# Optimization experiments

Hardware: AMD Instinct MI355X
Metric: run time of the kernel (lower is better)

The kernel has to match this reference:

```python
import jax, jax.numpy as jnp
import numpy as np

C_M, C_Z, C_H = 256, 128, 32
S, N = 128, 384
EPS = 1e-5


def setup_inputs() -> dict:
    key = jax.random.key(0)
    ks = jax.random.split(key, 8)
    sc = 1.0 / np.sqrt(C_M)
    return {
        "msa": jax.random.normal(ks[0], (S, N, C_M), dtype=jnp.float32),
        "ln_g": jnp.ones((C_M,), dtype=jnp.float32),
        "ln_b": jnp.zeros((C_M,), dtype=jnp.float32),
        "Wl": jax.random.uniform(ks[1], (C_M, C_H), jnp.float32, -sc, sc),
        "bl": jax.random.uniform(ks[2], (C_H,), jnp.float32, -sc, sc),
        "Wr": jax.random.uniform(ks[3], (C_M, C_H), jnp.float32, -sc, sc),
        "br": jax.random.uniform(ks[4], (C_H,), jnp.float32, -sc, sc),
        "Wo": jax.random.uniform(ks[5], (C_H * C_H, C_Z), jnp.float32, -1.0 / C_H, 1.0 / C_H),
        "bo": jax.random.uniform(ks[6], (C_Z,), jnp.float32, -1.0 / C_H, 1.0 / C_H),
    }


def _layernorm(x, g, b):
    mu = jnp.mean(x, axis=-1, keepdims=True)
    var = jnp.mean(jnp.square(x - mu), axis=-1, keepdims=True)
    return (x - mu) * jax.lax.rsqrt(var + EPS) * g + b


def reference(msa, ln_g, ln_b, Wl, bl, Wr, br, Wo, bo):
    s = msa.shape[0]
    m = _layernorm(msa, ln_g, ln_b)          # [s, n, c_m]
    left = m @ Wl + bl                        # [s, n, c_h]
    right = m @ Wr + br                       # [s, n, c_h]
    outer = jnp.einsum('sic,sjd->ijcd', left, right) / s  # [n, n, c_h, c_h]
    outer = outer.reshape(outer.shape[0], outer.shape[1], -1)
    return outer @ Wo + bo                    # [n, n, c_z]
```

## Files before the change

kernel.cpp:

```cpp
#include <hip/hip_runtime.h>
#include <hip/hip_bf16.h>

#define CM 256
#define CZ 128
#define CH 32
#define SS 128
#define NN 384

typedef short bf16x8 __attribute__((ext_vector_type(8)));
typedef float f32x4 __attribute__((ext_vector_type(4)));
typedef unsigned short us4 __attribute__((ext_vector_type(4)));
typedef unsigned short us8 __attribute__((ext_vector_type(8)));

__device__ __forceinline__ unsigned short f2bf(float f) {
    __hip_bfloat16 h = __float2bfloat16(f);
    return __builtin_bit_cast(unsigned short, h);
}

__device__ __forceinline__ void gl_lds16(const unsigned short* g, unsigned short* l) {
    __builtin_amdgcn_global_load_lds(
        (const __attribute__((address_space(1))) unsigned int*)g,
        (__attribute__((address_space(3))) unsigned int*)l,
        16, 0, 0);
}

__global__ __launch_bounds__(256) void k0_transpose(
    const float* __restrict__ Wo, const float* __restrict__ Wl, const float* __restrict__ Wr,
    unsigned short* __restrict__ WoF, unsigned short* __restrict__ WT) {
    int n = blockIdx.x;
    int base = n * 1024;
#pragma unroll
    for (int u = 0; u < 4; u++) {
        int w   = base + u * 256 + threadIdx.x;
        int e   = w & 7;
        int l   = (w >> 3) & 63;
        int zb  = (w >> 9) & 7;
        int cch = w >> 12;
        WoF[w] = f2bf(Wo[(size_t)(cch * 32 + (l >> 4) * 8 + e) * CZ + zb * 16 + (l & 15)]);
    }
    int k = threadIdx.x;
    if (n < 32) {
        WT[n * CM + k] = f2bf(Wl[(size_t)k * CH + n]);
    } else if (n < 64) {
        WT[32 * CM + (n - 32) * CM + k] = f2bf(Wr[(size_t)k * CH + (n - 32)]);
    }
}

__global__ __launch_bounds__(256, 2) void k1_ln_proj(
    const float* __restrict__ msa, const float* __restrict__ g, const float* __restrict__ bta,
    const unsigned short* __restrict__ WT, const float* __restrict__ bl, const float* __restrict__ br,
    unsigned short* __restrict__ Lt, unsigned short* __restrict__ Rt)
{
    __shared__ unsigned short A_lds[64 * 264];
    __shared__ unsigned short B_lds[64 * 264];

    const int i    = blockIdx.x;
    const int sh   = blockIdx.y;
    const int t    = threadIdx.x;
    const int wv   = t >> 6;
    const int lane = t & 63;
    const int lr   = lane & 15, lg = lane >> 4;

    const float4 gv = ((const float4*)g)[lane];
    const float4 bv = ((const float4*)bta)[lane];
#pragma unroll 4
    for (int r = 0; r < 16; r++) {
        int sl = wv * 16 + r;
        int s  = sh * 64 + sl;
        float4 v = ((const float4*)(msa + ((size_t)s * NN + i) * CM))[lane];
        float sum = v.x + v.y + v.z + v.w;
        float sq  = v.x * v.x + v.y * v.y + v.z * v.z + v.w * v.w;
#pragma unroll
        for (int off = 32; off >= 1; off >>= 1) {
            sum += __shfl_xor(sum, off, 64);
            sq  += __shfl_xor(sq, off, 64);
        }
        float mu = sum * (1.f / CM);
        float rs = rsqrtf(sq * (1.f / CM) - mu * mu + 1e-5f);
        us4 pk;
        pk[0] = f2bf((v.x - mu) * rs * gv.x + bv.x);
        pk[1] = f2bf((v.y - mu) * rs * gv.y + bv.y);
        pk[2] = f2bf((v.z - mu) * rs * gv.z + bv.z);
        pk[3] = f2bf((v.w - mu) * rs * gv.w + bv.w);
        *(us4*)&A_lds[sl * 264 + lane * 4] = pk;
    }
#pragma unroll
    for (int u = 0; u < 8; u++) {
        int id = u * 256 + t;
        *(us8*)&B_lds[(id >> 5) * 264 + (id & 31) * 8] = *(const us8*)&WT[id * 8];
    }
    __syncthreads();

    const int m0 = (wv >> 1) * 32;
    const int n0 = (wv & 1) * 32;
    f32x4 acc[2][2];
#pragma unroll
    for (int a = 0; a < 2; a++)
#pragma unroll
        for (int b = 0; b < 2; b++) acc[a][b] = (f32x4){0.f, 0.f, 0.f, 0.f};

#pragma unroll
    for (int ks = 0; ks < 8; ks++) {
        int ko = ks * 32 + lg * 8;
        bf16x8 a0 = *(const bf16x8*)&A_lds[(m0 + lr) * 264 + ko];
        bf16x8 a1 = *(const bf16x8*)&A_lds[(m0 + 16 + lr) * 264 + ko];
        bf16x8 b0 = *(const bf16x8*)&B_lds[(n0 + lr) * 264 + ko];
        bf16x8 b1 = *(const bf16x8*)&B_lds[(n0 + 16 + lr) * 264 + ko];
        acc[0][0] = __builtin_amdgcn_mfma_f32_16x16x32_bf16(a0, b0, acc[0][0], 0, 0, 0);
        acc[0][1] = __builtin_amdgcn_mfma_f32_16x16x32_bf16(a0, b1, acc[0][1], 0, 0, 0);
        acc[1][0] = __builtin_amdgcn_mfma_f32_16x16x32_bf16(a1, b0, acc[1][0], 0, 0, 0);
        acc[1][1] = __builtin_amdgcn_mfma_f32_16x16x32_bf16(a1, b1, acc[1][1], 0, 0, 0);
    }

    const bool isL = (n0 == 0);
    const float scale = isL ? 0.0078125f : 1.f;
#pragma unroll
    for (int mt = 0; mt < 2; mt++)
#pragma unroll
        for (int nt = 0; nt < 2; nt++) {
            int ch = (n0 + nt * 16 + lr) & 31;
            float bias = isL ? bl[ch] : br[ch];
            us4 pk;
#pragma unroll
            for (int rg = 0; rg < 4; rg++)
                pk[rg] = f2bf((acc[mt][nt][rg] + bias) * scale);
            unsigned short* dst = (isL ? Lt : Rt) + (size_t)(i * CH + ch) * SS
                                  + sh * 64 + m0 + mt * 16 + lg * 4;
            *(us4*)dst = pk;
        }
}

#define TI 8
#define TJ 8
#define P1_B_OFF 65536
#define OH1_OFF  65536
#define K2_LDS   139264

#define FRAG(base, row, o) \
    (*(const bf16x8*)((base) + (((o) & 8) << 11) + (row) * 64 + ((((o) & 7) ^ ((row) & 7)) << 3)))

__global__ __launch_bounds__(512, 2) void k2_fused(
    const unsigned short* __restrict__ Lt, const unsigned short* __restrict__ Rt,
    const unsigned short* __restrict__ WoF, const float* __restrict__ bo,
    float* __restrict__ out)
{
    extern __shared__ char smem[];
    unsigned short* A = (unsigned short*)(smem);
    unsigned short* B = (unsigned short*)(smem + P1_B_OFF);

    const int i0 = blockIdx.x * TI;
    const int j0 = blockIdx.y * TJ;
    const int t  = threadIdx.x;
    const int wv = t >> 6, lane = t & 63;
    const int lr = lane & 15, lg = lane >> 4;

    const unsigned short* gA = Lt + (size_t)i0 * CH * SS;
    const unsigned short* gB = Rt + (size_t)j0 * CH * SS;

    auto stage_half = [&](const unsigned short* gS, unsigned short* lS, int h) {
#pragma unroll
        for (int p = 0; p < 4; p++) {
            int q = wv * 4 + p;
            int d = q * 64 + lane;
            int row = d >> 3, ow = d & 7;
            const unsigned short* src = gS + row * 128 + (h * 8 + (ow ^ (row & 7))) * 8;
            gl_lds16(src, lS + h * 16384 + q * 512);
        }
    };

    stage_half(gA, A, 0);
    stage_half(gB, B, 0);
    asm volatile("s_waitcnt vmcnt(0)" ::: "memory");
    __syncthreads();
    stage_half(gA, A, 1);
    stage_half(gB, B, 1);

    const int m0  = (wv >> 2) * 128;
    const int n0w = (wv & 3) * 64;

    f32x4 accE[4][4], accO[4][4];
#pragma unroll
    for (int a = 0; a < 4; a++)
#pragma unroll
        for (int b = 0; b < 4; b++) {
            accE[a][b] = (f32x4){0.f, 0.f, 0.f, 0.f};
            accO[a][b] = (f32x4){0.f, 0.f, 0.f, 0.f};
        }

#pragma unroll
    for (int ks = 0; ks < 2; ks++) {
        int o = ks * 4 + lg;
        bf16x8 af[8], bfr[4];
#pragma unroll
        for (int mt = 0; mt < 8; mt++) af[mt]  = FRAG(A, m0 + mt * 16 + lr, o);
#pragma unroll
        for (int nt = 0; nt < 4; nt++) bfr[nt] = FRAG(B, n0w + nt * 16 + lr, o);
#pragma unroll
        for (int mt = 0; mt < 8; mt++)
#pragma unroll
            for (int nt = 0; nt < 4; nt++) {
                if (mt & 1)
                    accO[mt >> 1][nt] = __builtin_amdgcn_mfma_f32_16x16x32_bf16(bfr[nt], af[mt], accO[mt >> 1][nt], 0, 0, 0);
                else
                    accE[mt >> 1][nt] = __builtin_amdgcn_mfma_f32_16x16x32_bf16(bfr[nt], af[mt], accE[mt >> 1][nt], 0, 0, 0);
            }
    }
    asm volatile("s_waitcnt vmcnt(0)" ::: "memory");
    __syncthreads();
#pragma unroll
    for (int ks = 2; ks < 4; ks++) {
        int o = ks * 4 + lg;
        bf16x8 af[8], bfr[4];
#pragma unroll
        for (int mt = 0; mt < 8; mt++) af[mt]  = FRAG(A, m0 + mt * 16 + lr, o);
#pragma unroll
        for (int nt = 0; nt < 4; nt++) bfr[nt] = FRAG(B, n0w + nt * 16 + lr, o);
#pragma unroll
        for (int mt = 0; mt < 8; mt++)
#pragma unroll
            for (int nt = 0; nt < 4; nt++) {
                if (mt & 1)
                    accO[mt >> 1][nt] = __builtin_amdgcn_mfma_f32_16x16x32_bf16(bfr[nt], af[mt], accO[mt >> 1][nt], 0, 0, 0);
                else
                    accE[mt >> 1][nt] = __builtin_amdgcn_mfma_f32_16x16x32_bf16(bfr[nt], af[mt], accE[mt >> 1][nt], 0, 0, 0);
            }
    }
    __syncthreads();

    const int zsl = wv & 1, ksl = wv >> 1;

    bf16x8 wbuf[2][4];
#pragma unroll
    for (int bi = 0; bi < 4; bi++)
        wbuf[0][bi] = *(const bf16x8*)&WoF[(((size_t)(0 * 4 + ksl) * 8 + zsl * 4 + bi) * 64 + lane) * 8];
#pragma unroll
    for (int bi = 0; bi < 4; bi++)
        wbuf[1][bi] = *(const bf16x8*)&WoF[(((size_t)(1 * 4 + ksl) * 8 + zsl * 4 + bi) * 64 + lane) * 8];

    {
        unsigned short* Oh0 = (unsigned short*)smem;
        unsigned short* Oh1 = (unsigned short*)(smem + OH1_OFF);
#pragma unroll
        for (int mh = 0; mh < 4; mh++) {
            int iiw  = (wv >> 2) * 4 + mh;
            int rowH = iiw * 16 + lr;
            int okey = (rowH ^ (rowH >> 4)) & 7;
#pragma unroll
            for (int nt = 0; nt < 4; nt++) {
                int colBase = n0w + nt * 16 + lg * 4;
                int chk = (colBase >> 3) ^ okey;
                int off = rowH * 256 + chk * 8 + (lg & 1) * 4;
                us4 pkE, pkO;
#pragma unroll
                for (int rg = 0; rg < 4; rg++) {
                    pkE[rg] = f2bf(accE[mh][nt][rg]);
                    pkO[rg] = f2bf(accO[mh][nt][rg]);
                }
                *(us4*)&Oh0[off] = pkE;
                *(us4*)&Oh1[off] = pkO;
            }
        }
    }
    __syncthreads();

    f32x4 acc2[4][4];
#pragma unroll
    for (int a = 0; a < 4; a++)
#pragma unroll
        for (int b = 0; b < 4; b++) acc2[a][b] = (f32x4){0.f, 0.f, 0.f, 0.f};

#pragma unroll
    for (int c = 0; c < 8; c++) {
        const int cch = c * 4 + ksl;
        const int hh  = cch >> 4;
        const int cH  = cch & 15;
        const unsigned short* OhX = (const unsigned short*)(smem + (hh ? OH1_OFF : 0));

        bf16x8 af2[4];
#pragma unroll
        for (int ai = 0; ai < 4; ai++) {
            int rowH = (ai * 2 + ((lane >> 3) & 1)) * 16 + cH;
            int okey = (rowH ^ (rowH >> 4)) & 7;
            int chk  = (((lane & 7) * 4 + lg) ^ okey);
            af2[ai] = *(const bf16x8*)&OhX[rowH * 256 + chk * 8];
        }
#pragma unroll
        for (int ai = 0; ai < 4; ai++)
#pragma unroll
            for (int bi = 0; bi < 4; bi++)
                acc2[ai][bi] = __builtin_amdgcn_mfma_f32_16x16x32_bf16(af2[ai], wbuf[c & 1][bi], acc2[ai][bi], 0, 0, 0);

        if (c < 6) {
            int cchn = (c + 2) * 4 + ksl;
#pragma unroll
            for (int bi = 0; bi < 4; bi++)
                wbuf[c & 1][bi] = *(const bf16x8*)&WoF[(((size_t)cchn * 8 + zsl * 4 + bi) * 64 + lane) * 8];
        }
    }
    __syncthreads();

    float* RB = (float*)smem;
#pragma unroll
    for (int ai = 0; ai < 4; ai++)
#pragma unroll
        for (int bi = 0; bi < 4; bi++) {
            int z  = zsl * 64 + bi * 16 + lr;
            int pr = ai * 16 + lg * 4;
            *(f32x4*)&RB[ksl * 8704 + z * 68 + pr] = acc2[ai][bi];
        }
    __syncthreads();

    {
        int z = t >> 2, pq = t & 3;
        float bz = bo[z];
#pragma unroll
        for (int u = 0; u < 4; u++) {
            int p0r = pq * 16 + u * 4;
            f32x4 s = (f32x4){0.f, 0.f, 0.f, 0.f};
#pragma unroll
            for (int ks2 = 0; ks2 < 4; ks2++)
                s += *(const f32x4*)&RB[ks2 * 8704 + z * 68 + p0r];
#pragma unroll
            for (int e = 0; e < 4; e++) {
                int p = p0r + e;
                out[((size_t)(i0 + (p >> 3)) * NN + (j0 + (p & 7))) * CZ + z] = s[e] + bz;
            }
        }
    }
}

extern "C" void kernel_launch(void* const* d_in, const int* in_sizes, int n_in,
                              void* d_out, int out_size, void* d_ws, size_t ws_size,
                              hipStream_t stream) {
    const float* msa  = (const float*)d_in[0];
    const float* ln_g = (const float*)d_in[1];
    const float* ln_b = (const float*)d_in[2];
    const float* Wl   = (const float*)d_in[3];
    const float* bl   = (const float*)d_in[4];
    const float* Wr   = (const float*)d_in[5];
    const float* br   = (const float*)d_in[6];
    const float* Wo   = (const float*)d_in[7];
    const float* bo   = (const float*)d_in[8];
    float* out = (float*)d_out;

    unsigned short* Lt  = (unsigned short*)d_ws;
    unsigned short* Rt  = Lt + (size_t)NN * CH * SS;
    unsigned short* WoF = Rt + (size_t)NN * CH * SS;
    unsigned short* WT  = WoF + (size_t)CZ * CH * CH;

    hipFuncSetAttribute((const void*)k2_fused,
                        hipFuncAttributeMaxDynamicSharedMemorySize, K2_LDS);

    k0_transpose<<<dim3(CZ), dim3(256), 0, stream>>>(Wo, Wl, Wr, WoF, WT);
    k1_ln_proj<<<dim3(NN, 2), dim3(256), 0, stream>>>(msa, ln_g, ln_b, WT, bl, br, Lt, Rt);
    k2_fused<<<dim3(NN / TI, NN / TJ), dim3(512), K2_LDS, stream>>>(Lt, Rt, WoF, bo, out);
}
```

Before: 203.1 us.

## Make k2 persistent over nine tiles with register-prefetched next-tile inputs

The fused outer-product/projection kernel now launches 256 persistent blocks. Each block loops over 9 consecutive (i,j) tiles instead of one block per tile. The next tile's L/R slices are loaded into registers during the second GEMM and written to LDS after the epilogue, replacing the async global_load_lds staging. This targets launch/tail overhead and hides global-load latency, but adds register pressure, extra barriers per tile, and leaves roughly 256 blocks on 256 CUs with little latency hiding. The LN/projection loop unroll is also raised from 4 to 8.

```diff
diff --git a/kernel.cpp b/kernel.cpp
--- a/kernel.cpp
+++ b/kernel.cpp
@@ -15,13 +15,6 @@
 __device__ __forceinline__ unsigned short f2bf(float f) {
     __hip_bfloat16 h = __float2bfloat16(f);
     return __builtin_bit_cast(unsigned short, h);
-}
-
-__device__ __forceinline__ void gl_lds16(const unsigned short* g, unsigned short* l) {
-    __builtin_amdgcn_global_load_lds(
-        (const __attribute__((address_space(1))) unsigned int*)g,
-        (__attribute__((address_space(3))) unsigned int*)l,
-        16, 0, 0);
 }
 
 __global__ __launch_bounds__(256) void k0_transpose(
@@ -63,7 +56,7 @@
 
     const float4 gv = ((const float4*)g)[lane];
     const float4 bv = ((const float4*)bta)[lane];
-#pragma unroll 4
+#pragma unroll 8
     for (int r = 0; r < 16; r++) {
         int sl = wv * 16 + r;
         int s  = sh * 64 + sl;
@@ -132,6 +125,7 @@
 
 #define TI 8
 #define TJ 8
+#define TPB 9
 #define P1_B_OFF 65536
 #define OH1_OFF  65536
 #define K2_LDS   139264
@@ -148,184 +142,194 @@
     unsigned short* A = (unsigned short*)(smem);
     unsigned short* B = (unsigned short*)(smem + P1_B_OFF);
 
-    const int i0 = blockIdx.x * TI;
-    const int j0 = blockIdx.y * TJ;
     const int t  = threadIdx.x;
     const int wv = t >> 6, lane = t & 63;
     const int lr = lane & 15, lg = lane >> 4;
-
-    const unsigned short* gA = Lt + (size_t)i0 * CH * SS;
-    const unsigned short* gB = Rt + (size_t)j0 * CH * SS;
-
-    auto stage_half = [&](const unsigned short* gS, unsigned short* lS, int h) {
-#pragma unroll
-        for (int p = 0; p < 4; p++) {
-            int q = wv * 4 + p;
-            int d = q * 64 + lane;
-            int row = d >> 3, ow = d & 7;
-            const unsigned short* src = gS + row * 128 + (h * 8 + (ow ^ (row & 7))) * 8;
-            gl_lds16(src, lS + h * 16384 + q * 512);
-        }
-    };
-
-    stage_half(gA, A, 0);
-    stage_half(gB, B, 0);
-    asm volatile("s_waitcnt vmcnt(0)" ::: "memory");
-    __syncthreads();
-    stage_half(gA, A, 1);
-    stage_half(gB, B, 1);
-
+    const int zsl = wv & 1, ksl = wv >> 1;
     const int m0  = (wv >> 2) * 128;
     const int n0w = (wv & 3) * 64;
 
-    f32x4 accE[4][4], accO[4][4];
-#pragma unroll
-    for (int a = 0; a < 4; a++)
-#pragma unroll
-        for (int b = 0; b < 4; b++) {
-            accE[a][b] = (f32x4){0.f, 0.f, 0.f, 0.f};
-            accO[a][b] = (f32x4){0.f, 0.f, 0.f, 0.f};
-        }
-
-#pragma unroll
-    for (int ks = 0; ks < 2; ks++) {
-        int o = ks * 4 + lg;
-        bf16x8 af[8], bfr[4];
-#pragma unroll
-        for (int mt = 0; mt < 8; mt++) af[mt]  = FRAG(A, m0 + mt * 16 + lr, o);
-#pragma unroll
-        for (int nt = 0; nt < 4; nt++) bfr[nt] = FRAG(B, n0w + nt * 16 + lr, o);
-#pragma unroll
-        for (int mt = 0; mt < 8; mt++)
-#pragma unroll
-            for (int nt = 0; nt < 4; nt++) {
-                if (mt & 1)
-                    accO[mt >> 1][nt] = __builtin_amdgcn_mfma_f32_16x16x32_bf16(bfr[nt], af[mt], accO[mt >> 1][nt], 0, 0, 0);
-                else
-                    accE[mt >> 1][nt] = __builtin_amdgcn_mfma_f32_16x16x32_bf16(bfr[nt], af[mt], accE[mt >> 1][nt], 0, 0, 0);
-            }
-    }
-    asm volatile("s_waitcnt vmcnt(0)" ::: "memory");
+    int srow[8], skc[8], sdst[8];
+#pragma unroll
+    for (int u = 0; u < 8; u++) {
+        int c = u * 512 + t;
+        srow[u] = c >> 4;
+        skc[u]  = c & 15;
+        sdst[u] = (skc[u] >> 3) * 16384 + srow[u] * 64 + ((skc[u] & 7) ^ (srow[u] & 7)) * 8;
+    }
+
+    us8 rA[8], rB[8];
+    int tid = blockIdx.x * TPB;
+
+    {
+        const unsigned short* gA = Lt + (size_t)((tid / 48) * TI) * CH * SS;
+        const unsigned short* gB = Rt + (size_t)((tid % 48) * TJ) * CH * SS;
+#pragma unroll
+        for (int u = 0; u < 8; u++) {
+            rA[u] = *(const us8*)(gA + srow[u] * 128 + skc[u] * 8);
+            rB[u] = *(const us8*)(gB + srow[u] * 128 + skc[u] * 8);
+        }
+#pragma unroll
+        for (int u = 0; u < 8; u++) {
+            *(us8*)(A + sdst[u]) = rA[u];
+            *(us8*)(B + sdst[u]) = rB[u];
+        }
+    }
     __syncthreads();
-#pragma unroll
-    for (int ks = 2; ks < 4; ks++) {
-        int o = ks * 4 + lg;
-        bf16x8 af[8], bfr[4];
-#pragma unroll
-        for (int mt = 0; mt < 8; mt++) af[mt]  = FRAG(A, m0 + mt * 16 + lr, o);
-#pragma unroll
-        for (int nt = 0; nt < 4; nt++) bfr[nt] = FRAG(B, n0w + nt * 16 + lr, o);
-#pragma unroll
-        for (int mt = 0; mt < 8; mt++)
-#pragma unroll
-            for (int nt = 0; nt < 4; nt++) {
-                if (mt & 1)
-                    accO[mt >> 1][nt] = __builtin_amdgcn_mfma_f32_16x16x32_bf16(bfr[nt], af[mt], accO[mt >> 1][nt], 0, 0, 0);
-                else
-                    accE[mt >> 1][nt] = __builtin_amdgcn_mfma_f32_16x16x32_bf16(bfr[nt], af[mt], accE[mt >> 1][nt], 0, 0, 0);
-            }
-    }
-    __syncthreads();
-
-    const int zsl = wv & 1, ksl = wv >> 1;
-
-    bf16x8 wbuf[2][4];
-#pragma unroll
-    for (int bi = 0; bi < 4; bi++)
-        wbuf[0][bi] = *(const bf16x8*)&WoF[(((size_t)(0 * 4 + ksl) * 8 + zsl * 4 + bi) * 64 + lane) * 8];
-#pragma unroll
-    for (int bi = 0; bi < 4; bi++)
-        wbuf[1][bi] = *(const bf16x8*)&WoF[(((size_t)(1 * 4 + ksl) * 8 + zsl * 4 + bi) * 64 + lane) * 8];
-
-    {
-        unsigned short* Oh0 = (unsigned short*)smem;
-        unsigned short* Oh1 = (unsigned short*)(smem + OH1_OFF);
-#pragma unroll
-        for (int mh = 0; mh < 4; mh++) {
-            int iiw  = (wv >> 2) * 4 + mh;
-            int rowH = iiw * 16 + lr;
-            int okey = (rowH ^ (rowH >> 4)) & 7;
-#pragma unroll
-            for (int nt = 0; nt < 4; nt++) {
-                int colBase = n0w + nt * 16 + lg * 4;
-                int chk = (colBase >> 3) ^ okey;
-                int off = rowH * 256 + chk * 8 + (lg & 1) * 4;
-                us4 pkE, pkO;
-#pragma unroll
-                for (int rg = 0; rg < 4; rg++) {
-                    pkE[rg] = f2bf(accE[mh][nt][rg]);
-                    pkO[rg] = f2bf(accO[mh][nt][rg]);
+
+    for (int tt = 0; tt < TPB; tt++, tid++) {
+        const int i0 = (tid / 48) * TI;
+        const int j0 = (tid % 48) * TJ;
+
+        f32x4 accE[4][4], accO[4][4];
+#pragma unroll
+        for (int a = 0; a < 4; a++)
+#pragma unroll
+            for (int b = 0; b < 4; b++) {
+                accE[a][b] = (f32x4){0.f, 0.f, 0.f, 0.f};
+                accO[a][b] = (f32x4){0.f, 0.f, 0.f, 0.f};
+            }
+
+#pragma unroll
+        for (int ks = 0; ks < 4; ks++) {
+            int o = ks * 4 + lg;
+            bf16x8 af[8], bfr[4];
+#pragma unroll
+            for (int mt = 0; mt < 8; mt++) af[mt]  = FRAG(A, m0 + mt * 16 + lr, o);
+#pragma unroll
+            for (int nt = 0; nt < 4; nt++) bfr[nt] = FRAG(B, n0w + nt * 16 + lr, o);
+#pragma unroll
+            for (int mt = 0; mt < 8; mt++)
+#pragma unroll
+                for (int nt = 0; nt < 4; nt++) {
+                    if (mt & 1)
+                        accO[mt >> 1][nt] = __builtin_amdgcn_mfma_f32_16x16x32_bf16(bfr[nt], af[mt], accO[mt >> 1][nt], 0, 0, 0);
+                    else
+                        accE[mt >> 1][nt] = __builtin_amdgcn_mfma_f32_16x16x32_bf16(bfr[nt], af[mt], accE[mt >> 1][nt], 0, 0, 0);
                 }
-                *(us4*)&Oh0[off] = pkE;
-                *(us4*)&Oh1[off] = pkO;
-            }
-        }
-    }
-    __syncthreads();
-
-    f32x4 acc2[4][4];
-#pragma unroll
-    for (int a = 0; a < 4; a++)
-#pragma unroll
-        for (int b = 0; b < 4; b++) acc2[a][b] = (f32x4){0.f, 0.f, 0.f, 0.f};
-
-#pragma unroll
-    for (int c = 0; c < 8; c++) {
-        const int cch = c * 4 + ksl;
-        const int hh  = cch >> 4;
-        const int cH  = cch & 15;
-        const unsigned short* OhX = (const unsigned short*)(smem + (hh ? OH1_OFF : 0));
-
-        bf16x8 af2[4];
-#pragma unroll
-        for (int ai = 0; ai < 4; ai++) {
-            int rowH = (ai * 2 + ((lane >> 3) & 1)) * 16 + cH;
-            int okey = (rowH ^ (rowH >> 4)) & 7;
-            int chk  = (((lane & 7) * 4 + lg) ^ okey);
-            af2[ai] = *(const bf16x8*)&OhX[rowH * 256 + chk * 8];
-        }
+        }
+
+        bf16x8 wbuf[2][4];
+#pragma unroll
+        for (int bi = 0; bi < 4; bi++)
+            wbuf[0][bi] = *(const bf16x8*)&WoF[(((size_t)(0 * 4 + ksl) * 8 + zsl * 4 + bi) * 64 + lane) * 8];
+#pragma unroll
+        for (int bi = 0; bi < 4; bi++)
+            wbuf[1][bi] = *(const bf16x8*)&WoF[(((size_t)(1 * 4 + ksl) * 8 + zsl * 4 + bi) * 64 + lane) * 8];
+
+        __syncthreads();
+
+        {
+            unsigned short* Oh0 = (unsigned short*)smem;
+            unsigned short* Oh1 = (unsigned short*)(smem + OH1_OFF);
+#pragma unroll
+            for (int mh = 0; mh < 4; mh++) {
+                int iiw  = (wv >> 2) * 4 + mh;
+                int rowH = iiw * 16 + lr;
+                int okey = (rowH ^ (rowH >> 4)) & 7;
+#pragma unroll
+                for (int nt = 0; nt < 4; nt++) {
+                    int colBase = n0w + nt * 16 + lg * 4;
+                    int chk = (colBase >> 3) ^ okey;
+                    int off = rowH * 256 + chk * 8 + (lg & 1) * 4;
+                    us4 pkE, pkO;
+#pragma unroll
+                    for (int rg = 0; rg < 4; rg++) {
+                        pkE[rg] = f2bf(accE[mh][nt][rg]);
+                        pkO[rg] = f2bf(accO[mh][nt][rg]);
+                    }
+                    *(us4*)&Oh0[off] = pkE;
+                    *(us4*)&Oh1[off] = pkO;
+                }
+            }
+        }
+        __syncthreads();
+
+        if (tt < TPB - 1) {
+            int ntid = tid + 1;
+            const unsigned short* gA = Lt + (size_t)((ntid / 48) * TI) * CH * SS;
+            const unsigned short* gB = Rt + (size_t)((ntid % 48) * TJ) * CH * SS;
+#pragma unroll
+            for (int u = 0; u < 8; u++) {
+                rA[u] = *(const us8*)(gA + srow[u] * 128 + skc[u] * 8);
+                rB[u] = *(const us8*)(gB + srow[u] * 128 + skc[u] * 8);
+            }
+        }
+
+        f32x4 acc2[4][4];
+#pragma unroll
+        for (int a = 0; a < 4; a++)
+#pragma unroll
+            for (int b = 0; b < 4; b++) acc2[a][b] = (f32x4){0.f, 0.f, 0.f, 0.f};
+
+#pragma unroll
+        for (int c = 0; c < 8; c++) {
+            const int cch = c * 4 + ksl;
+            const int hh  = cch >> 4;
+            const int cH  = cch & 15;
+            const unsigned short* OhX = (const unsigned short*)(smem + (hh ? OH1_OFF : 0));
+
+            bf16x8 af2[4];
+#pragma unroll
+            for (int ai = 0; ai < 4; ai++) {
+                int rowH = (ai * 2 + ((lane >> 3) & 1)) * 16 + cH;
+                int okey = (rowH ^ (rowH >> 4)) & 7;
+                int chk  = (((lane & 7) * 4 + lg) ^ okey);
+                af2[ai] = *(const bf16x8*)&OhX[rowH * 256 + chk * 8];
+            }
+#pragma unroll
+            for (int ai = 0; ai < 4; ai++)
+#pragma unroll
+                for (int bi = 0; bi < 4; bi++)
+                    acc2[ai][bi] = __builtin_amdgcn_mfma_f32_16x16x32_bf16(af2[ai], wbuf[c & 1][bi], acc2[ai][bi], 0, 0, 0);
+
+            if (c < 6) {
+                int cchn = (c + 2) * 4 + ksl;
+#pragma unroll
+                for (int bi = 0; bi < 4; bi++)
+                    wbuf[c & 1][bi] = *(const bf16x8*)&WoF[(((size_t)cchn * 8 + zsl * 4 + bi) * 64 + lane) * 8];
+            }
+        }
+        __syncthreads();
+
+        float* RB = (float*)smem;
 #pragma unroll
         for (int ai = 0; ai < 4; ai++)
 #pragma unroll
-            for (int bi = 0; bi < 4; bi++)
-                acc2[ai][bi] = __builtin_amdgcn_mfma_f32_16x16x32_bf16(af2[ai], wbuf[c & 1][bi], acc2[ai][bi], 0, 0, 0);
-
-        if (c < 6) {
-            int cchn = (c + 2) * 4 + ksl;
-#pragma unroll
-            for (int bi = 0; bi < 4; bi++)
-                wbuf[c & 1][bi] = *(const bf16x8*)&WoF[(((size_t)cchn * 8 + zsl * 4 + bi) * 64 + lane) * 8];
-        }
-    }
-    __syncthreads();
-
-    float* RB = (float*)smem;
-#pragma unroll
-    for (int ai = 0; ai < 4; ai++)
-#pragma unroll
-        for (int bi = 0; bi < 4; bi++) {
-            int z  = zsl * 64 + bi * 16 + lr;
-            int pr = ai * 16 + lg * 4;
-            *(f32x4*)&RB[ksl * 8704 + z * 68 + pr] = acc2[ai][bi];
-        }
-    __syncthreads();
-
-    {
-        int z = t >> 2, pq = t & 3;
-        float bz = bo[z];
-#pragma unroll
-        for (int u = 0; u < 4; u++) {
-            int p0r = pq * 16 + u * 4;
-            f32x4 s = (f32x4){0.f, 0.f, 0.f, 0.f};
-#pragma unroll
-            for (int ks2 = 0; ks2 < 4; ks2++)
-                s += *(const f32x4*)&RB[ks2 * 8704 + z * 68 + p0r];
-#pragma unroll
-            for (int e = 0; e < 4; e++) {
-                int p = p0r + e;
-                out[((size_t)(i0 + (p >> 3)) * NN + (j0 + (p & 7))) * CZ + z] = s[e] + bz;
-            }
-        }
+            for (int bi = 0; bi < 4; bi++) {
+                int z  = zsl * 64 + bi * 16 + lr;
+                int pr = ai * 16 + lg * 4;
+                *(f32x4*)&RB[ksl * 8704 + z * 68 + pr] = acc2[ai][bi];
+            }
+        __syncthreads();
+
+        {
+            int z = t >> 2, pq = t & 3;
+            float bz = bo[z];
+#pragma unroll
+            for (int u = 0; u < 4; u++) {
+                int p0r = pq * 16 + u * 4;
+                f32x4 s = (f32x4){0.f, 0.f, 0.f, 0.f};
+#pragma unroll
+                for (int ks2 = 0; ks2 < 4; ks2++)
+                    s += *(const f32x4*)&RB[ks2 * 8704 + z * 68 + p0r];
+#pragma unroll
+                for (int e = 0; e < 4; e++) {
+                    int p = p0r + e;
+                    out[((size_t)(i0 + (p >> 3)) * NN + (j0 + (p & 7))) * CZ + z] = s[e] + bz;
+                }
+            }
+        }
+        __syncthreads();
+
+        if (tt < TPB - 1) {
+#pragma unroll
+            for (int u = 0; u < 8; u++) {
+                *(us8*)(A + sdst[u]) = rA[u];
+                *(us8*)(B + sdst[u]) = rB[u];
+            }
+        }
+        __syncthreads();
     }
 }
 
@@ -353,5 +357,5 @@
 
     k0_transpose<<<dim3(CZ), dim3(256), 0, stream>>>(Wo, Wl, Wr, WoF, WT);
     k1_ln_proj<<<dim3(NN, 2), dim3(256), 0, stream>>>(msa, ln_g, ln_b, WT, bl, br, Lt, Rt);
-    k2_fused<<<dim3(NN / TI, NN / TJ), dim3(512), K2_LDS, stream>>>(Lt, Rt, WoF, bo, out);
-}
+    k2_fused<<<dim3(256), dim3(512), K2_LDS, stream>>>(Lt, Rt, WoF, bo, out);
+}
```

Result: slower. 472.2 us (+132.5%).
